# Kernel optimization log

Measured on AMD Instinct MI355X. Metric: run time of the kernel, lower is better.

Reference implementation:

```python
import jax, jax.numpy as jnp
import numpy as np
from jax import lax

N_HEADS = 10
F_IN = 78
F_OUT = 78           # per-head GAT output dim
HID = N_HEADS * F_OUT  # 780
NEG_SLOPE = 0.2
NUM_GRAPHS = 1024
N_NODES = 40960
N_EDGES = 163840
VOCAB = 26           # CHARPROTLEN + 1
EMB = 128
NFILT = 32
LOUT = 121           # 128 - 8 + 1


def setup_inputs() -> dict:
    key = jax.random.key(0)
    ks = jax.random.split(key, 24)
    d = {}
    d['x'] = jax.random.normal(ks[0], (N_NODES, F_IN), jnp.float32)
    d['edge_index'] = jax.random.randint(ks[1], (2, N_EDGES), 0, N_NODES, jnp.int64)
    d['batch'] = jnp.sort(jax.random.randint(ks[2], (N_NODES,), 0, NUM_GRAPHS, jnp.int64))
    d['target'] = jax.random.randint(ks[3], (NUM_GRAPHS, 1000), 0, VOCAB, jnp.int64)
    s = 0.05
    d['gat_W'] = jax.random.normal(ks[4], (F_IN, HID), jnp.float32) * s
    d['gat_att_src'] = jax.random.normal(ks[5], (N_HEADS, F_OUT), jnp.float32) * s
    d['gat_att_dst'] = jax.random.normal(ks[6], (N_HEADS, F_OUT), jnp.float32) * s
    d['gat_bias'] = jnp.zeros((HID,), jnp.float32)
    d['gcn_W'] = jax.random.normal(ks[7], (HID, HID), jnp.float32) * s
    d['gcn_bias'] = jnp.zeros((HID,), jnp.float32)
    d['fc_g1_W'] = jax.random.normal(ks[8], (2 * HID, 1500), jnp.float32) * s
    d['fc_g1_b'] = jnp.zeros((1500,), jnp.float32)
    d['fc_g2_W'] = jax.random.normal(ks[9], (1500, 128), jnp.float32) * s
    d['fc_g2_b'] = jnp.zeros((128,), jnp.float32)
    d['embed'] = jax.random.normal(ks[10], (VOCAB, EMB), jnp.float32) * s
    d['conv_xt_W'] = jax.random.normal(ks[11], (NFILT, 1000, 8), jnp.float32) * s
    d['conv_xt_b'] = jnp.zeros((NFILT,), jnp.float32)
    d['fc1_xt_W'] = jax.random.normal(ks[12], (NFILT * LOUT, 128), jnp.float32) * s
    d['fc1_xt_b'] = jnp.zeros((128,), jnp.float32)
    d['fc1_W'] = jax.random.normal(ks[13], (256, 1024), jnp.float32) * s
    d['fc1_b'] = jnp.zeros((1024,), jnp.float32)
    d['fc2_W'] = jax.random.normal(ks[14], (1024, 512), jnp.float32) * s
    d['fc2_b'] = jnp.zeros((512,), jnp.float32)
    d['out_W'] = jax.random.normal(ks[15], (512, 1), jnp.float32) * s
    d['out_b'] = jnp.zeros((1,), jnp.float32)
    return d


def _segment_softmax(logits, seg, num_segments):
    m = jax.ops.segment_max(logits, seg, num_segments=num_segments)
    m = jnp.where(jnp.isfinite(m), m, 0.0)
    e = jnp.exp(logits - m[seg])
    s = jax.ops.segment_sum(e, seg, num_segments=num_segments)
    return e / (s[seg] + 1e-16)


def reference(x, edge_index, batch, target, gat_W, gat_att_src, gat_att_dst,
              gat_bias, gcn_W, gcn_bias, fc_g1_W, fc_g1_b, fc_g2_W, fc_g2_b,
              embed, conv_xt_W, conv_xt_b, fc1_xt_W, fc1_xt_b, fc1_W, fc1_b,
              fc2_W, fc2_b, out_W, out_b):
    N = x.shape[0]
    # add self loops (PyG default for both GATConv and GCNConv)
    loops = jnp.arange(N, dtype=edge_index.dtype)
    src = jnp.concatenate([edge_index[0], loops])
    dst = jnp.concatenate([edge_index[1], loops])
    # --- GATConv(78 -> 78, heads=10, concat) ---
    h = (x @ gat_W).reshape(N, N_HEADS, F_OUT)              # [N,10,78]
    a_src = jnp.einsum('nhf,hf->nh', h, gat_att_src)        # [N,10]
    a_dst = jnp.einsum('nhf,hf->nh', h, gat_att_dst)
    logits = jax.nn.leaky_relu(a_src[src] + a_dst[dst], NEG_SLOPE)  # [E',10]
    alpha = _segment_softmax(logits, dst, N)                # softmax over in-edges per dst/head
    agg = jax.ops.segment_sum(h[src] * alpha[:, :, None], dst, num_segments=N)
    x1 = jax.nn.relu(agg.reshape(N, HID) + gat_bias)        # [N,780]
    # --- GCNConv(780 -> 780) with sym normalization ---
    h2 = x1 @ gcn_W
    deg = jax.ops.segment_sum(jnp.ones_like(dst, dtype=h2.dtype), dst, num_segments=N)
    dinv = jnp.where(deg > 0, deg ** -0.5, 0.0)
    norm = dinv[src] * dinv[dst]                            # [E']
    agg2 = jax.ops.segment_sum(h2[src] * norm[:, None], dst, num_segments=N)
    x2 = jax.nn.relu(agg2 + gcn_bias)                       # [N,780]
    # --- global max + mean pool per graph ---
    gmax = jax.ops.segment_max(x2, batch, num_segments=NUM_GRAPHS)
    cnt = jax.ops.segment_sum(jnp.ones((N,), x2.dtype), batch, num_segments=NUM_GRAPHS)
    gmean = jax.ops.segment_sum(x2, batch, num_segments=NUM_GRAPHS) / jnp.maximum(cnt, 1.0)[:, None]
    g = jnp.concatenate([gmax, gmean], axis=1)              # [B,1560]
    g = jax.nn.relu(g @ fc_g1_W + fc_g1_b)
    g = g @ fc_g2_W + fc_g2_b                               # [B,128] (dropout = identity, eval)
    # --- protein branch ---
    e = embed[target]                                       # [B,1000,128]
    conv = lax.conv_general_dilated(e, conv_xt_W, (1,), 'VALID',
                                    dimension_numbers=('NCH', 'OIH', 'NCH'))
    conv = conv + conv_xt_b[None, :, None]                  # [B,32,121]
    xt = conv.reshape(conv.shape[0], NFILT * LOUT) @ fc1_xt_W + fc1_xt_b
    # --- joint head ---
    xc = jnp.concatenate([g, xt], axis=1)                   # [B,256]
    xc = jax.nn.relu(xc @ fc1_W + fc1_b)
    xc = jax.nn.relu(xc @ fc2_W + fc2_b)
    return xc @ out_W + out_b                               # [B,1]
```

## Files before the change

kernel.cpp:

```cpp
#include <hip/hip_runtime.h>

typedef __attribute__((ext_vector_type(4))) float f32x4;
typedef __attribute__((ext_vector_type(8))) short bf16x8;
typedef __attribute__((ext_vector_type(8))) unsigned short u16x8;
typedef unsigned short u16;

#define HID 780
#define NH 10
#define FO 78

__device__ inline u16 f2b(float f) {
  unsigned u = __float_as_uint(f);
  unsigned r = (u + 0x7fff + ((u >> 16) & 1)) >> 16;
  return (u16)r;
}
__device__ inline float b2f(u16 b) { return __uint_as_float(((unsigned)b) << 16); }

__device__ inline void gld16(const u16* g, u16* l) {
  __builtin_amdgcn_global_load_lds(
      (const __attribute__((address_space(1))) unsigned int*)g,
      (__attribute__((address_space(3))) unsigned int*)l, 16, 0, 0);
}

__device__ inline int swz_bid() {
  int gx = gridDim.x, gy = gridDim.y, gz = gridDim.z;
  int nwg = gx * gy * gz;
  int bid = (blockIdx.z * gy + blockIdx.y) * gx + blockIdx.x;
  if ((nwg & 7) == 0) bid = (bid & 7) * (nwg >> 3) + (bid >> 3);
  return bid;
}

__device__ __forceinline__ void gemm_core(const u16* __restrict__ A,
    const u16* __restrict__ BT, u16* __restrict__ C, float* __restrict__ att_out,
    int Ncols, int KP, int ldc, int bx, int by,
    u16 (*As)[4096], u16 (*Bs)[4096])
{
  const int tid = threadIdx.x;
  const int row0 = by << 7, col0 = bx << 7;
  const int l = tid & 63, wid = tid >> 6;
  const int wr = wid >> 1, wc = wid & 1;
  const int lr = l & 15, lk = l >> 4;
  const int c0 = (wid << 6) + l, c1 = 256 + c0;
  const u16* gA0 = A + (size_t)(row0 + (c0 >> 2)) * KP + ((c0 & 3) << 3);
  const u16* gA1 = A + (size_t)(row0 + (c1 >> 2)) * KP + ((c1 & 3) << 3);
  const u16* gB0 = BT + (size_t)(col0 + (c0 >> 2)) * KP + ((c0 & 3) << 3);
  const u16* gB1 = BT + (size_t)(col0 + (c1 >> 2)) * KP + ((c1 & 3) << 3);
  const int d0 = (wid << 6) << 3, d1 = (256 + (wid << 6)) << 3;

  f32x4 acc[4][4];
#pragma unroll
  for (int i = 0; i < 4; ++i)
#pragma unroll
    for (int j = 0; j < 4; ++j) acc[i][j] = (f32x4){0.f, 0.f, 0.f, 0.f};

  gld16(gA0, &As[0][d0]); gld16(gA1, &As[0][d1]);
  gld16(gB0, &Bs[0][d0]); gld16(gB1, &Bs[0][d1]);
  __syncthreads();

  int cur = 0;
  for (int k0 = 0; k0 < KP; k0 += 32) {
    if (k0 + 32 < KP) {
      int nx = cur ^ 1, kn = k0 + 32;
      gld16(gA0 + kn, &As[nx][d0]); gld16(gA1 + kn, &As[nx][d1]);
      gld16(gB0 + kn, &Bs[nx][d0]); gld16(gB1 + kn, &Bs[nx][d1]);
    }
    const u16* Ac = As[cur];
    const u16* Bc = Bs[cur];
    bf16x8 af[4], bfr[4];
#pragma unroll
    for (int fm = 0; fm < 4; ++fm)
      af[fm] = *(const bf16x8*)&Ac[((wr * 64 + fm * 16 + lr) << 5) + (lk << 3)];
#pragma unroll
    for (int fn = 0; fn < 4; ++fn)
      bfr[fn] = *(const bf16x8*)&Bc[((wc * 64 + fn * 16 + lr) << 5) + (lk << 3)];
#pragma unroll
    for (int fm = 0; fm < 4; ++fm)
#pragma unroll
      for (int fn = 0; fn < 4; ++fn)
        acc[fm][fn] = __builtin_amdgcn_mfma_f32_16x16x32_bf16(af[fm], bfr[fn], acc[fm][fn], 0, 0, 0);
    __syncthreads();
    cur ^= 1;
  }
#pragma unroll
  for (int fm = 0; fm < 4; ++fm)
#pragma unroll
    for (int fn = 0; fn < 4; ++fn) {
      int col = col0 + wc * 64 + fn * 16 + lr;
      f32x4 v = acc[fm][fn];
      int rbase = row0 + wr * 64 + fm * 16 + lk * 4;
      if (col < Ncols) {
#pragma unroll
        for (int j = 0; j < 4; ++j)
          C[(size_t)(rbase + j) * ldc + col] = f2b(v[j]);
      } else {
        if (att_out != nullptr && col < Ncols + 20) {
          int c = col - Ncols;
#pragma unroll
          for (int j = 0; j < 4; ++j)
            att_out[(size_t)(rbase + j) * 20 + c] = v[j];
        }
        if (col < ldc) {
#pragma unroll
          for (int j = 0; j < 4; ++j) C[(size_t)(rbase + j) * ldc + col] = 0;
        }
      }
    }
}

__global__ __launch_bounds__(256) void gemm_mfma(const u16* __restrict__ A,
    const u16* __restrict__ BT, u16* __restrict__ C, float* __restrict__ att_out,
    int Ncols, int KP, int ldc)
{
  __shared__ u16 As[2][4096];
  __shared__ u16 Bs[2][4096];
  int t = swz_bid();
  gemm_core(A, BT, C, att_out, Ncols, KP, ldc, t % gridDim.x, t / gridDim.x, As, Bs);
}

__global__ __launch_bounds__(256) void gemm_dual(
    const u16* __restrict__ A1, const u16* __restrict__ B1, u16* __restrict__ C1,
    float* __restrict__ att1, int N1, int K1, int l1, int gx1, int nb1,
    const u16* __restrict__ A2, const u16* __restrict__ B2, u16* __restrict__ C2,
    int N2, int K2, int l2, int gx2)
{
  __shared__ u16 As[2][4096];
  __shared__ u16 Bs[2][4096];
  int bi = blockIdx.x;
  if (bi < nb1) {
    int t = bi;
    if ((nb1 & 7) == 0) t = (bi & 7) * (nb1 >> 3) + (bi >> 3);
    gemm_core(A1, B1, C1, att1, N1, K1, l1, t % gx1, t / gx1, As, Bs);
  } else {
    int nb2 = gridDim.x - nb1, b2 = bi - nb1;
    int t = b2;
    if ((nb2 & 7) == 0) t = (b2 & 7) * (nb2 >> 3) + (b2 >> 3);
    gemm_core(A2, B2, C2, nullptr, N2, K2, l2, t % gx2, t / gx2, As, Bs);
  }
}

__device__ __forceinline__ void sk_core(const u16* __restrict__ A,
    const u16* __restrict__ BT, float* __restrict__ C,
    int Ncols, int KP, int kchunk, int bx, int by, int bz,
    u16 (*As)[4096], u16 (*Bs)[4096])
{
  const int tid = threadIdx.x;
  const int row0 = by << 7, col0 = bx << 7;
  const int kbeg = bz * kchunk;
  const int kend = min(KP, kbeg + kchunk);
  const int l = tid & 63, wid = tid >> 6;
  const int wr = wid >> 1, wc = wid & 1;
  const int lr = l & 15, lk = l >> 4;
  const int c0 = (wid << 6) + l, c1 = 256 + c0;
  const u16* gA0 = A + (size_t)(row0 + (c0 >> 2)) * KP + ((c0 & 3) << 3) + kbeg;
  const u16* gA1 = A + (size_t)(row0 + (c1 >> 2)) * KP + ((c1 & 3) << 3) + kbeg;
  const u16* gB0 = BT + (size_t)(col0 + (c0 >> 2)) * KP + ((c0 & 3) << 3) + kbeg;
  const u16* gB1 = BT + (size_t)(col0 + (c1 >> 2)) * KP + ((c1 & 3) << 3) + kbeg;
  const int d0 = (wid << 6) << 3, d1 = (256 + (wid << 6)) << 3;

  f32x4 acc[4][4];
#pragma unroll
  for (int i = 0; i < 4; ++i)
#pragma unroll
    for (int j = 0; j < 4; ++j) acc[i][j] = (f32x4){0.f, 0.f, 0.f, 0.f};

  gld16(gA0, &As[0][d0]); gld16(gA1, &As[0][d1]);
  gld16(gB0, &Bs[0][d0]); gld16(gB1, &Bs[0][d1]);
  __syncthreads();

  int cur = 0;
  for (int k0 = kbeg; k0 < kend; k0 += 32) {
    if (k0 + 32 < kend) {
      int nx = cur ^ 1, kn = k0 + 32 - kbeg;
      gld16(gA0 + kn, &As[nx][d0]); gld16(gA1 + kn, &As[nx][d1]);
      gld16(gB0 + kn, &Bs[nx][d0]); gld16(gB1 + kn, &Bs[nx][d1]);
    }
    const u16* Ac = As[cur];
    const u16* Bc = Bs[cur];
    bf16x8 af[4], bfr[4];
#pragma unroll
    for (int fm = 0; fm < 4; ++fm)
      af[fm] = *(const bf16x8*)&Ac[((wr * 64 + fm * 16 + lr) << 5) + (lk << 3)];
#pragma unroll
    for (int fn = 0; fn < 4; ++fn)
      bfr[fn] = *(const bf16x8*)&Bc[((wc * 64 + fn * 16 + lr) << 5) + (lk << 3)];
#pragma unroll
    for (int fm = 0; fm < 4; ++fm)
#pragma unroll
      for (int fn = 0; fn < 4; ++fn)
        acc[fm][fn] = __builtin_amdgcn_mfma_f32_16x16x32_bf16(af[fm], bfr[fn], acc[fm][fn], 0, 0, 0);
    __syncthreads();
    cur ^= 1;
  }
#pragma unroll
  for (int fm = 0; fm < 4; ++fm)
#pragma unroll
    for (int fn = 0; fn < 4; ++fn) {
      int col = col0 + wc * 64 + fn * 16 + lr;
      if (col < Ncols) {
        f32x4 v = acc[fm][fn];
        int rbase = row0 + wr * 64 + fm * 16 + lk * 4;
#pragma unroll
        for (int j = 0; j < 4; ++j)
          atomicAdd(&C[(size_t)(rbase + j) * Ncols + col], v[j]);
      }
    }
}

__global__ __launch_bounds__(256) void gemm_sk(const u16* __restrict__ A,
    const u16* __restrict__ BT, float* __restrict__ C,
    int Ncols, int KP, int kchunk)
{
  __shared__ u16 As[2][4096];
  __shared__ u16 Bs[2][4096];
  int t = swz_bid();
  int bx = t % gridDim.x;
  int by = (t / gridDim.x) % gridDim.y;
  int bz = t / (gridDim.x * gridDim.y);
  sk_core(A, BT, C, Ncols, KP, kchunk, bx, by, bz, As, Bs);
}

__global__ __launch_bounds__(256) void gemm_sk_dual(
    const u16* __restrict__ A1, const u16* __restrict__ B1, float* __restrict__ C1,
    int N1, int K1, int kc1, int gx1, int gy1, int nb1,
    const u16* __restrict__ A2, const u16* __restrict__ B2, float* __restrict__ C2,
    int N2, int K2, int kc2, int gx2, int gy2)
{
  __shared__ u16 As[2][4096];
  __shared__ u16 Bs[2][4096];
  int bi = blockIdx.x;
  if (bi < nb1) {
    int t = bi;
    if ((nb1 & 7) == 0) t = (bi & 7) * (nb1 >> 3) + (bi >> 3);
    sk_core(A1, B1, C1, N1, K1, kc1, t % gx1, (t / gx1) % gy1, t / (gx1 * gy1), As, Bs);
  } else {
    int nb2 = gridDim.x - nb1, b2 = bi - nb1;
    int t = b2;
    if ((nb2 & 7) == 0) t = (b2 & 7) * (nb2 >> 3) + (b2 >> 3);
    sk_core(A2, B2, C2, N2, K2, kc2, t % gx2, (t / gx2) % gy2, t / (gx2 * gy2), As, Bs);
  }
}

template<bool RELU>
__global__ void bias_act_pad(const float* __restrict__ Cf,
    const float* __restrict__ bias, u16* __restrict__ out,
    int M, int N, int padTo, int ldco)
{
  int idx = blockIdx.x * 256 + threadIdx.x;
  if (idx >= M * padTo) return;
  int r = idx / padTo, c = idx - r * padTo;
  if (c < N) {
    float v = Cf[(size_t)r * N + c] + bias[c];
    if (RELU) v = v > 0.f ? v : 0.f;
    out[(size_t)r * ldco + c] = f2b(v);
  } else {
    out[(size_t)r * ldco + c] = 0;
  }
}

__global__ void bias_dual(const float* __restrict__ C1, const float* __restrict__ b1,
    u16* __restrict__ o1, int M1, int N1, int p1, int l1,
    const float* __restrict__ C2, const float* __restrict__ b2,
    u16* __restrict__ o2, int M2, int N2, int p2, int l2)
{
  int idx = blockIdx.x * 256 + threadIdx.x;
  int t1 = M1 * p1;
  if (idx < t1) {
    int r = idx / p1, c = idx - r * p1;
    if (c < N1) o1[(size_t)r * l1 + c] = f2b(C1[(size_t)r * N1 + c] + b1[c]);
    else o1[(size_t)r * l1 + c] = 0;
    return;
  }
  idx -= t1;
  if (idx >= M2 * p2) return;
  int r = idx / p2, c = idx - r * p2;
  if (c < N2) {
    float v = C2[(size_t)r * N2 + c] + b2[c];
    v = v > 0.f ? v : 0.f;
    o2[(size_t)r * l2 + c] = f2b(v);
  } else {
    o2[(size_t)r * l2 + c] = 0;
  }
}

__device__ inline void wtile(const float* __restrict__ W, u16* __restrict__ WT,
    int K, int Ncol, int KP, int NP, int bx, int by, int skip_lo, int skip_hi,
    u16 (*tbuf)[33])
{
  int tn0 = bx << 5, tk0 = by << 5;
  int lx = threadIdx.x & 31, ly = threadIdx.x >> 5;
#pragma unroll
  for (int r = 0; r < 32; r += 8) {
    int k = tk0 + ly + r, n = tn0 + lx;
    tbuf[ly + r][lx] = (k < K && n < Ncol) ? f2b(W[(size_t)k * Ncol + n]) : (u16)0;
  }
  __syncthreads();
#pragma unroll
  for (int r = 0; r < 32; r += 8) {
    int n = tn0 + ly + r, k = tk0 + lx;
    if (n < NP && k < KP && !(n >= skip_lo && n < skip_hi))
      WT[(size_t)n * KP + k] = tbuf[lx][ly + r];
  }
}

__global__ __launch_bounds__(256) void prep_all(
    const float* __restrict__ x, u16* __restrict__ xb,
    const float* __restrict__ gat_W, u16* __restrict__ wt1,
    const float* __restrict__ gcn_W, u16* __restrict__ wt2,
    const float* __restrict__ fcg1_W, u16* __restrict__ wtg1,
    const float* __restrict__ fcg2_W, u16* __restrict__ wtg2,
    const float* __restrict__ fc1xt_W, u16* __restrict__ wtxt,
    const float* __restrict__ fc1_W, u16* __restrict__ wtf1,
    const float* __restrict__ fc2_W, u16* __restrict__ wtf2,
    const float* __restrict__ convW, u16* __restrict__ wtc,
    const float* __restrict__ asv, const float* __restrict__ adv,
    const int* __restrict__ tgt, u16* __restrict__ Ind,
    const int* __restrict__ ei, int* __restrict__ cnt, int N, int E)
{
  __shared__ u16 tbuf[32][33];
  __shared__ unsigned char tl[1000];
  int bi = blockIdx.x, tid = threadIdx.x;
  const int s0 = (N * 96 + 255) / 256;
  if (bi < s0) {
    int idx = bi * 256 + tid;
    if (idx < N * 96) {
      int r = idx / 96, c = idx - r * 96;
      xb[idx] = (c < FO) ? f2b(x[(size_t)r * FO + c]) : (u16)0;
    }
    return;
  }
  bi -= s0;
  if (bi < 84)   { wtile(gat_W,  wt1,  FO,   HID,  96,   896,  bi % 28, bi / 28, 780, 800, tbuf); return; }
  bi -= 84;
  if (bi < 700)  { wtile(gcn_W,  wt2,  HID,  HID,  800,  896,  bi % 28, bi / 28, 1 << 30, 0, tbuf); return; }
  bi -= 700;
  if (bi < 2352) { wtile(fcg1_W, wtg1, 1560, 1500, 1568, 1536, bi % 48, bi / 48, 1 << 30, 0, tbuf); return; }
  bi -= 2352;
  if (bi < 188)  { wtile(fcg2_W, wtg2, 1500, 128,  1504, 128,  bi % 4,  bi / 4,  1 << 30, 0, tbuf); return; }
  bi -= 188;
  if (bi < 484)  { wtile(fc1xt_W, wtxt, 3872, 128, 3872, 128,  bi % 4,  bi / 4,  1 << 30, 0, tbuf); return; }
  bi -= 484;
  if (bi < 256)  { wtile(fc1_W,  wtf1, 256,  1024, 256,  1024, bi % 32, bi / 32, 1 << 30, 0, tbuf); return; }
  bi -= 256;
  if (bi < 512)  { wtile(fc2_W,  wtf2, 1024, 512,  1024, 512,  bi % 16, bi / 16, 1 << 30, 0, tbuf); return; }
  bi -= 512;
  if (bi < 1024) {
    int idx = bi * 256 + tid;
    int ok = idx >> 10, c = idx & 1023;
    int o = ok >> 3, k = ok & 7;
    wtc[idx] = (c < 1000) ? f2b(convW[(size_t)o * 8000 + c * 8 + k]) : (u16)0;
    return;
  }
  bi -= 1024;
  if (bi < 20) {
    int j = bi, k = tid;
    if (k >= 96) return;
    float s = 0.f;
    if (k < FO) {
      int h = (j < 10) ? j : j - 10;
      const float* av = ((j < 10) ? asv : adv) + h * FO;
      const float* wr = gat_W + (size_t)k * HID + h * FO;
      for (int f = 0; f < FO; ++f) s += wr[f] * av[f];
    }
    wt1[(size_t)(HID + j) * 96 + k] = f2b(s);
    return;
  }
  bi -= 20;
  if (bi < 1024) {
    int b = bi;
    for (int i = tid; i < 1000; i += 256) tl[i] = (unsigned char)tgt[b * 1000 + i];
    __syncthreads();
    u16* out = Ind + (size_t)b * 26 * 1024;
    for (int ci = tid; ci < 26 * 128; ci += 256) {
      int v = ci >> 7, c0 = (ci & 127) << 3;
      u16x8 w;
#pragma unroll
      for (int j = 0; j < 8; ++j) {
        int c = c0 + j;
        w[j] = (c < 1000 && tl[c] == v) ? (u16)0x3F80 : (u16)0;
      }
      *(u16x8*)(out + v * 1024 + c0) = w;
    }
    return;
  }
  bi -= 1024;
  {
    int e = bi * 256 + tid;
    if (e >= E + N) return;
    int dst = (e < E) ? ei[E + e] : (e - E);
    atomicAdd(&cnt[dst], 1);
  }
}

__global__ __launch_bounds__(1024) void scan1(const int* __restrict__ cnt,
    int* __restrict__ offs, float* __restrict__ dinv, int* __restrict__ bsum, int N)
{
  __shared__ int sc[1024];
  int b = blockIdx.x, tid = threadIdx.x;
  int g = b * 1024 + tid;
  int c = (g < N) ? cnt[g] : 0;
  sc[tid] = c;
  __syncthreads();
  for (int off = 1; off < 1024; off <<= 1) {
    int v = sc[tid];
    int add = (tid >= off) ? sc[tid - off] : 0;
    __syncthreads();
    sc[tid] = v + add;
    __syncthreads();
  }
  if (g < N) {
    offs[g] = sc[tid] - c;
    dinv[g] = c > 0 ? rsqrtf((float)c) : 0.f;
  }
  if (tid == 1023) bsum[b] = sc[1023];
}

__global__ __launch_bounds__(1024) void scan2(int* __restrict__ offs,
    const int* __restrict__ bsum, int N, int nblk)
{
  int b = blockIdx.x, tid = threadIdx.x;
  int base = 0;
  for (int j = 0; j < b; ++j) base += bsum[j];
  int g = b * 1024 + tid;
  if (g < N && b > 0) offs[g] += base;
  if (b == nblk - 1 && tid == 1023) offs[N] = base + bsum[b];
}

__global__ void fill_csr(const int* __restrict__ ei, int E, int N,
    const int* __restrict__ offs, int* __restrict__ fillpos, int* __restrict__ csr_src)
{
  int e = blockIdx.x * 256 + threadIdx.x;
  if (e >= E + N) return;
  int src, dst;
  if (e < E) { src = ei[e]; dst = ei[E + e]; }
  else { src = e - E; dst = e - E; }
  int p = offs[dst] + atomicAdd(&fillpos[dst], 1);
  csr_src[p] = src;
}

#define CH 48
__global__ __launch_bounds__(64) void gat_gather(const u16* __restrict__ h,
    const float* __restrict__ att,
    const int* __restrict__ offs, const int* __restrict__ csr_src,
    const float* __restrict__ gat_bias, u16* __restrict__ x1b)
{
  int n = blockIdx.x, lane = threadIdx.x;
  int o0 = offs[n], deg = offs[n + 1] - o0;
  __shared__ float ad[NH], ssum[NH];
  __shared__ float wbuf[CH][NH];
  __shared__ int slist[CH];
  if (lane < NH) { ad[lane] = att[n * 20 + 10 + lane]; ssum[lane] = 0.f; }
  const int s0 = lane, s1 = 64 + lane;
  const bool a1 = s1 < 100;
  int hA0 = min((s0 * 8) / FO, NH - 1), bb0 = FO * ((s0 * 8) / FO + 1) - s0 * 8;
  int hB0 = min((s0 * 8) / FO + 1, NH - 1);
  int hA1 = min((s1 * 8) / FO, NH - 1), bb1 = FO * ((s1 * 8) / FO + 1) - s1 * 8;
  int hB1 = min((s1 * 8) / FO + 1, NH - 1);
  float acc0[8], acc1[8];
#pragma unroll
  for (int j = 0; j < 8; ++j) { acc0[j] = 0.f; acc1[j] = 0.f; }
  __syncthreads();

  for (int e0 = 0; e0 < deg; e0 += CH) {
    int ce = min(CH, deg - e0);
    for (int idx = lane; idx < ce * NH; idx += 64) {
      int e = idx / NH, hd = idx - e * NH;
      int s = csr_src[o0 + e0 + e];
      float l = att[s * 20 + hd] + ad[hd];
      l = l > 0.f ? l : 0.2f * l;
      float w = __expf(l);
      wbuf[e][hd] = w;
      atomicAdd(&ssum[hd], w);
    }
    for (int idx = lane; idx < ce; idx += 64) slist[idx] = csr_src[o0 + e0 + idx];
    __syncthreads();
    for (int e = 0; e < ce; ++e) {
      const u16* hs = h + (size_t)slist[e] * 800;
      u16x8 v0 = *(const u16x8*)(hs + s0 * 8);
      float wA0 = wbuf[e][hA0], wB0 = wbuf[e][hB0];
#pragma unroll
      for (int j = 0; j < 8; ++j)
        acc0[j] += (j < bb0 ? wA0 : wB0) * b2f(v0[j]);
      if (a1) {
        u16x8 v1 = *(const u16x8*)(hs + s1 * 8);
        float wA1 = wbuf[e][hA1], wB1 = wbuf[e][hB1];
#pragma unroll
        for (int j = 0; j < 8; ++j)
          acc1[j] += (j < bb1 ? wA1 : wB1) * b2f(v1[j]);
      }
    }
    __syncthreads();
  }
  float iA0 = 1.f / (ssum[hA0] + 1e-16f), iB0 = 1.f / (ssum[hB0] + 1e-16f);
  u16x8 o0v;
#pragma unroll
  for (int j = 0; j < 8; ++j) {
    int f = s0 * 8 + j;
    float v = acc0[j] * (j < bb0 ? iA0 : iB0) + gat_bias[f];
    o0v[j] = f2b(v > 0.f ? v : 0.f);
  }
  *(u16x8*)(x1b + (size_t)n * 800 + s0 * 8) = o0v;
  if (a1) {
    float iA1 = 1.f / (ssum[hA1] + 1e-16f), iB1 = 1.f / (ssum[hB1] + 1e-16f);
    u16x8 o1v;
#pragma unroll
    for (int j = 0; j < 8; ++j) {
      int f = s1 * 8 + j;
      if (f < HID) {
        float v = acc1[j] * (j < bb1 ? iA1 : iB1) + gat_bias[f];
        o1v[j] = f2b(v > 0.f ? v : 0.f);
      } else o1v[j] = 0;
    }
    *(u16x8*)(x1b + (size_t)n * 800 + s1 * 8) = o1v;
  }
}

__global__ __launch_bounds__(256) void gcn_pool(const u16* __restrict__ h2,
    const int* __restrict__ offs, const int* __restrict__ csr_src,
    const float* __restrict__ dinv, const float* __restrict__ gcn_bias,
    const int* __restrict__ batch, int N, u16* __restrict__ gb)
{
  int gi = blockIdx.x, tid = threadIdx.x;
  int grp = tid >> 6, lane = tid & 63;
  __shared__ int se[2];
  __shared__ float smx[HID];
  __shared__ float ssm[HID];
  for (int f = tid; f < HID; f += 256) { smx[f] = 0.f; ssm[f] = 0.f; }
  if (tid < 2) {
    int target = gi + tid;
    int lo = 0, hi = N;
    while (lo < hi) { int mid = (lo + hi) >> 1; if (batch[mid] < target) lo = mid + 1; else hi = mid; }
    se[tid] = lo;
  }
  __syncthreads();
  int s = se[0], e = se[1];
  const int s0 = lane, s1 = 64 + lane;
  const bool a1 = s1 < 100;
  float bv0[8], bv1[8];
#pragma unroll
  for (int j = 0; j < 8; ++j) {
    int f0 = s0 * 8 + j, f1 = s1 * 8 + j;
    bv0[j] = gcn_bias[f0];
    bv1[j] = (a1 && f1 < HID) ? gcn_bias[f1] : 0.f;
  }
  float mx0[8], sm0[8], mx1[8], sm1[8];
#pragma unroll
  for (int j = 0; j < 8; ++j) { mx0[j] = 0.f; sm0[j] = 0.f; mx1[j] = 0.f; sm1[j] = 0.f; }

  for (int n = s + grp; n < e; n += 4) {
    int o0 = offs[n], deg = offs[n + 1] - o0;
    float dn = dinv[n];
    float acc0[8], acc1[8];
#pragma unroll
    for (int j = 0; j < 8; ++j) { acc0[j] = 0.f; acc1[j] = 0.f; }
    for (int eb = 0; eb < deg; eb += 64) {
      int ce = min(64, deg - eb);
      int   src_l = (lane < ce) ? csr_src[o0 + eb + lane] : 0;
      float c_l   = (lane < ce) ? dn * dinv[src_l] : 0.f;
      int   sc = __shfl(src_l, 0, 64);
      float cc = __shfl(c_l, 0, 64);
      const u16* hr = h2 + (size_t)sc * 800;
      u16x8 v0 = *(const u16x8*)(hr + s0 * 8);
      u16x8 v1 = a1 ? *(const u16x8*)(hr + s1 * 8) : v0;
      for (int ed = 0; ed < ce; ++ed) {
        u16x8 n0 = v0, n1 = v1;
        float nc = 0.f;
        if (ed + 1 < ce) {
          int ns = __shfl(src_l, ed + 1, 64);
          nc = __shfl(c_l, ed + 1, 64);
          const u16* nh = h2 + (size_t)ns * 800;
          n0 = *(const u16x8*)(nh + s0 * 8);
          if (a1) n1 = *(const u16x8*)(nh + s1 * 8);
        }
#pragma unroll
        for (int j = 0; j < 8; ++j) acc0[j] += cc * b2f(v0[j]);
        if (a1) {
#pragma unroll
          for (int j = 0; j < 8; ++j) acc1[j] += cc * b2f(v1[j]);
        }
        v0 = n0; v1 = n1; cc = nc;
      }
    }
#pragma unroll
    for (int j = 0; j < 8; ++j) {
      float v = acc0[j] + bv0[j];
      v = v > 0.f ? v : 0.f;
      mx0[j] = fmaxf(mx0[j], v); sm0[j] += v;
      float w = acc1[j] + bv1[j];
      w = w > 0.f ? w : 0.f;
      mx1[j] = fmaxf(mx1[j], w); sm1[j] += w;
    }
  }
#pragma unroll
  for (int j = 0; j < 8; ++j) {
    int f0 = s0 * 8 + j;
    atomicMax((unsigned*)&smx[f0], __float_as_uint(mx0[j]));
    atomicAdd(&ssm[f0], sm0[j]);
    int f1 = s1 * 8 + j;
    if (a1 && f1 < HID) {
      atomicMax((unsigned*)&smx[f1], __float_as_uint(mx1[j]));
      atomicAdd(&ssm[f1], sm1[j]);
    }
  }
  __syncthreads();
  float inv = 1.f / fmaxf((float)(e - s), 1.f);
  for (int f = tid; f < HID; f += 256) {
    gb[(size_t)gi * 1568 + f] = f2b(smx[f]);
    gb[(size_t)gi * 1568 + HID + f] = f2b(ssm[f] * inv);
  }
  if (tid < 8) gb[(size_t)gi * 1568 + 1560 + tid] = 0;
}

__global__ __launch_bounds__(256) void conv_xt(const u16* __restrict__ Aall,
    const float* __restrict__ embed, const float* __restrict__ cbias,
    u16* __restrict__ out)
{
  int b = blockIdx.x, tid = threadIdx.x;
  __shared__ __align__(16) float Al[6656];
  __shared__ __align__(16) float el[3360];
  const u16* Ab = Aall + (size_t)b * 6656;
  for (int i = tid; i < 6656; i += 256) Al[i] = b2f(Ab[i]);
  for (int i = tid; i < 3328; i += 256) el[i] = embed[i];
  if (tid < 32) el[3328 + tid] = 0.f;
  __syncthreads();
  for (int grp = tid; grp < 512; grp += 256) {
    int o = grp >> 4;
    int l0 = (grp & 15) << 3;
    float cb = cbias[o];
    float acc[8];
#pragma unroll
    for (int j = 0; j < 8; ++j) acc[j] = cb;
    for (int v = 0; v < 26; ++v) {
      const float* ap = &Al[v * 256 + (o << 3)];
      f32x4 a0 = *(const f32x4*)ap;
      f32x4 a1 = *(const f32x4*)(ap + 4);
      const float* ep = &el[v * 128 + l0];
      f32x4 e0 = *(const f32x4*)ep;
      f32x4 e1 = *(const f32x4*)(ep + 4);
      f32x4 e2 = *(const f32x4*)(ep + 8);
      f32x4 e3 = *(const f32x4*)(ep + 12);
      float a[8] = { a0[0], a0[1], a0[2], a0[3], a1[0], a1[1], a1[2], a1[3] };
      float e[16] = { e0[0], e0[1], e0[2], e0[3], e1[0], e1[1], e1[2], e1[3],
                      e2[0], e2[1], e2[2], e2[3], e3[0], e3[1], e3[2], e3[3] };
#pragma unroll
      for (int k = 0; k < 8; ++k)
#pragma unroll
        for (int j = 0; j < 8; ++j) acc[j] += a[k] * e[k + j];
    }
    int base = o * 121 + l0;
#pragma unroll
    for (int j = 0; j < 8; ++j)
      if (l0 + j < 121) out[(size_t)b * 3872 + base + j] = f2b(acc[j]);
  }
}

__global__ __launch_bounds__(256) void final_out(const u16* __restrict__ z2,
    const float* __restrict__ W, const float* __restrict__ bias, float* __restrict__ out)
{
  int row = blockIdx.x * 4 + (threadIdx.x >> 6);
  int lane = threadIdx.x & 63;
  const u16* zr = z2 + (size_t)row * 512;
  float s = 0.f;
  for (int i = lane; i < 512; i += 64) s += b2f(zr[i]) * W[i];
#pragma unroll
  for (int off = 32; off > 0; off >>= 1) s += __shfl_down(s, off, 64);
  if (lane == 0) out[row] = s + bias[0];
}

extern "C" void kernel_launch(void* const* d_in, const int* in_sizes, int n_in,
                              void* d_out, int out_size, void* d_ws, size_t ws_size,
                              hipStream_t stream)
{
  const float* x        = (const float*)d_in[0];
  const int*   ei       = (const int*)d_in[1];
  const int*   batch    = (const int*)d_in[2];
  const int*   tgt      = (const int*)d_in[3];
  const float* gat_W    = (const float*)d_in[4];
  const float* att_src  = (const float*)d_in[5];
  const float* att_dst  = (const float*)d_in[6];
  const float* gat_bias = (const float*)d_in[7];
  const float* gcn_W    = (const float*)d_in[8];
  const float* gcn_bias = (const float*)d_in[9];
  const float* fcg1_W   = (const float*)d_in[10];
  const float* fcg1_b   = (const float*)d_in[11];
  const float* fcg2_W   = (const float*)d_in[12];
  const float* fcg2_b   = (const float*)d_in[13];
  const float* embed    = (const float*)d_in[14];
  const float* convW    = (const float*)d_in[15];
  const float* convb    = (const float*)d_in[16];
  const float* fc1xt_W  = (const float*)d_in[17];
  const float* fc1xt_b  = (const float*)d_in[18];
  const float* fc1_W    = (const float*)d_in[19];
  const float* fc1_b    = (const float*)d_in[20];
  const float* fc2_W    = (const float*)d_in[21];
  const float* fc2_b    = (const float*)d_in[22];
  const float* out_W    = (const float*)d_in[23];
  const float* out_b    = (const float*)d_in[24];

  const int N = in_sizes[0] / FO;
  const int E = in_sizes[1] / 2;
  const int B = in_sizes[3] / 1000;
  const int ET = E + N;

  char* ws = (char*)d_ws;
  size_t off = 0;
  auto alloc = [&](size_t bytes) -> char* {
    char* p = ws + off;
    off = (off + bytes + 255) & ~(size_t)255;
    return p;
  };
  float* buf0  = (float*)alloc((size_t)N * HID * 4);
  float* buf1  = (float*)alloc((size_t)N * 800 * 2);
  u16*   Ab       = (u16*)alloc((size_t)26624 * 256 * 2);
  u16*   convflat = (u16*)alloc((size_t)1024 * 3872 * 2);
  u16*   wt1   = (u16*)alloc((size_t)896 * 96 * 2);
  u16*   wt2   = (u16*)alloc((size_t)896 * 800 * 2);
  u16*   wtg1  = (u16*)alloc((size_t)1536 * 1568 * 2);
  u16*   wtg2  = (u16*)alloc((size_t)128 * 1504 * 2);
  u16*   wtxt  = (u16*)alloc((size_t)128 * 3872 * 2);
  u16*   wtf1  = (u16*)alloc((size_t)1024 * 256 * 2);
  u16*   wtf2  = (u16*)alloc((size_t)512 * 1024 * 2);
  u16*   wtc   = (u16*)alloc((size_t)256 * 1024 * 2);
  float* att   = (float*)alloc((size_t)N * 20 * 4);
  int*   cnt   = (int*)alloc((size_t)N * 4);
  int*   offs  = (int*)alloc((size_t)(N + 1) * 4);
  int*   fillp = (int*)alloc((size_t)N * 4);
  int*   csr   = (int*)alloc((size_t)ET * 4);
  float* dinv  = (float*)alloc((size_t)N * 4);
  u16*   gb    = (u16*)alloc((size_t)B * 1568 * 2);
  int*   bsum  = (int*)alloc((size_t)64 * 4);

  u16*   xb    = (u16*)buf1;
  u16*   Ind   = (u16*)((char*)buf1 + (size_t)N * 96 * 2);
  u16*   x1b   = (u16*)buf1;
  u16*   hb    = (u16*)buf0;
  float* g1f = buf0;
  float* xtf = g1f + (size_t)1024 * 1500;
  float* g2f = xtf + (size_t)1024 * 128;
  float* z1f = g2f + (size_t)1024 * 128;
  float* z2f = z1f + (size_t)1024 * 1024;
  size_t skBytes = ((size_t)1024 * (1500 + 128 + 128 + 1024 + 512)) * 4;
  u16* g1b = (u16*)buf1;
  u16* xcb = g1b + (size_t)1024 * 1504;
  u16* z1b = xcb + (size_t)1024 * 256;
  u16* z2b = z1b + (size_t)1024 * 1024;

  hipMemsetAsync(cnt, 0, (size_t)N * 4, stream);
  hipMemsetAsync(fillp, 0, (size_t)N * 4, stream);

  int nbx = (N * 96 + 255) / 256;
  int nprep = nbx + 84 + 700 + 2352 + 188 + 484 + 256 + 512 + 1024 + 20 + 1024 + (ET + 255) / 256;
  prep_all<<<nprep, 256, 0, stream>>>(
      x, xb, gat_W, wt1, gcn_W, wt2, fcg1_W, wtg1, fcg2_W, wtg2,
      fc1xt_W, wtxt, fc1_W, wtf1, fc2_W, wtf2, convW, wtc,
      att_src, att_dst, tgt, Ind, ei, cnt, N, E);

  int nb1 = 7 * (N / 128);
  int nb2 = 2 * (26624 / 128);
  gemm_dual<<<nb1 + nb2, 256, 0, stream>>>(
      xb, wt1, hb, att, HID, 96, 800, 7, nb1,
      Ind, wtc, Ab, 256, 1024, 256, 2);

  int nblk = (N + 1023) / 1024;
  scan1<<<nblk, 1024, 0, stream>>>(cnt, offs, dinv, bsum, N);
  scan2<<<nblk, 1024, 0, stream>>>(offs, bsum, N, nblk);
  conv_xt<<<B, 256, 0, stream>>>(Ab, embed, convb, convflat);
  fill_csr<<<(ET + 255) / 256, 256, 0, stream>>>(ei, E, N, offs, fillp, csr);

  gat_gather<<<N, 64, 0, stream>>>(hb, att, offs, csr, gat_bias, x1b);

  gemm_mfma<<<dim3(7, N / 128), 256, 0, stream>>>(x1b, wt2, hb, nullptr, HID, 800, 800);

  gcn_pool<<<B, 256, 0, stream>>>(hb, offs, csr, dinv, gcn_bias, batch, N, gb);

  hipMemsetAsync(g1f, 0, skBytes, stream);

  gemm_sk_dual<<<128 + 192, 256, 0, stream>>>(
      convflat, wtxt, xtf, 128, 3872, 256, 1, 8, 128,
      gb, wtg1, g1f, 1500, 1568, 800, 12, 8);
  int nbias = (B * 128 + B * 1504 + 255) / 256;
  bias_dual<<<nbias, 256, 0, stream>>>(
      xtf, fc1xt_b, xcb + 128, B, 128, 128, 256,
      g1f, fcg1_b, g1b, B, 1500, 1504, 1504);

  gemm_sk<<<dim3(1, B / 128, 8), 256, 0, stream>>>(g1b, wtg2, g2f, 128, 1504, 192);
  bias_act_pad<false><<<(B * 128 + 255) / 256, 256, 0, stream>>>(
      g2f, fcg2_b, xcb, B, 128, 128, 256);

  gemm_sk<<<dim3(8, B / 128, 2), 256, 0, stream>>>(xcb, wtf1, z1f, 1024, 256, 128);
  bias_act_pad<true><<<(B * 1024 + 255) / 256, 256, 0, stream>>>(
      z1f, fc1_b, z1b, B, 1024, 1024, 1024);

  gemm_sk<<<dim3(4, B / 128, 4), 256, 0, stream>>>(z1b, wtf2, z2f, 512, 1024, 256);
  bias_act_pad<true><<<(B * 512 + 255) / 256, 256, 0, stream>>>(
      z2f, fc2_b, z2b, B, 512, 512, 512);

  final_out<<<B / 4, 256, 0, stream>>>(z2b, out_W, out_b, (float*)d_out);
}
```

Measured before the change: 446.3 us.

## Triple-buffer MFMA GEMM LDS pipeline with explicit vmcnt waits

The bf16 MFMA GEMM core moves from a double-buffered global_load_lds scheme to a three-stage ring buffer. It prefetches three K-tiles ahead and uses explicit s_waitcnt vmcnt thresholds plus raw s_barrier, replacing the full __syncthreads after each step. The next loads are issued into the just-read buffer once its fragments are in registers, before the MFMAs run. The goal is to hide more global memory latency. The cost is 50% more LDS per block, which may lower occupancy, plus an extra barrier per iteration.

```diff
diff --git a/kernel.cpp b/kernel.cpp
--- a/kernel.cpp
+++ b/kernel.cpp
@@ -53,19 +53,25 @@
 #pragma unroll
     for (int j = 0; j < 4; ++j) acc[i][j] = (f32x4){0.f, 0.f, 0.f, 0.f};
 
-  gld16(gA0, &As[0][d0]); gld16(gA1, &As[0][d1]);
-  gld16(gB0, &Bs[0][d0]); gld16(gB1, &Bs[0][d1]);
-  __syncthreads();
-
-  int cur = 0;
-  for (int k0 = 0; k0 < KP; k0 += 32) {
-    if (k0 + 32 < KP) {
-      int nx = cur ^ 1, kn = k0 + 32;
-      gld16(gA0 + kn, &As[nx][d0]); gld16(gA1 + kn, &As[nx][d1]);
-      gld16(gB0 + kn, &Bs[nx][d0]); gld16(gB1 + kn, &Bs[nx][d1]);
-    }
-    const u16* Ac = As[cur];
-    const u16* Bc = Bs[cur];
+  const int niter = KP >> 5;
+  const int npre = niter < 3 ? niter : 3;
+  for (int t = 0; t < npre; ++t) {
+    int kk = t << 5;
+    gld16(gA0 + kk, &As[t][d0]); gld16(gA1 + kk, &As[t][d1]);
+    gld16(gB0 + kk, &Bs[t][d0]); gld16(gB1 + kk, &Bs[t][d1]);
+  }
+
+  int cb = 0;
+  for (int k = 0; k < niter; ++k) {
+    if (k + 2 < niter)      asm volatile("s_waitcnt vmcnt(8)" ::: "memory");
+    else if (k + 1 < niter) asm volatile("s_waitcnt vmcnt(4)" ::: "memory");
+    else                    asm volatile("s_waitcnt vmcnt(0)" ::: "memory");
+    __builtin_amdgcn_sched_barrier(0);
+    __builtin_amdgcn_s_barrier();
+    asm volatile("" ::: "memory");
+
+    const u16* Ac = As[cb];
+    const u16* Bc = Bs[cb];
     bf16x8 af[4], bfr[4];
 #pragma unroll
     for (int fm = 0; fm < 4; ++fm)
@@ -73,13 +79,25 @@
 #pragma unroll
     for (int fn = 0; fn < 4; ++fn)
       bfr[fn] = *(const bf16x8*)&Bc[((wc * 64 + fn * 16 + lr) << 5) + (lk << 3)];
+
+    if (k + 3 < niter) {
+      asm volatile("s_waitcnt lgkmcnt(0)" ::: "memory");
+      __builtin_amdgcn_sched_barrier(0);
+      __builtin_amdgcn_s_barrier();
+      asm volatile("" ::: "memory");
+      int kn = (k + 3) << 5;
+      gld16(gA0 + kn, &As[cb][d0]); gld16(gA1 + kn, &As[cb][d1]);
+      gld16(gB0 + kn, &Bs[cb][d0]); gld16(gB1 + kn, &Bs[cb][d1]);
+      __builtin_amdgcn_sched_barrier(0);
+    }
+
 #pragma unroll
     for (int fm = 0; fm < 4; ++fm)
 #pragma unroll
       for (int fn = 0; fn < 4; ++fn)
         acc[fm][fn] = __builtin_amdgcn_mfma_f32_16x16x32_bf16(af[fm], bfr[fn], acc[fm][fn], 0, 0, 0);
-    __syncthreads();
-    cur ^= 1;
+
+    cb = (cb == 2) ? 0 : cb + 1;
   }
 #pragma unroll
   for (int fm = 0; fm < 4; ++fm)
@@ -111,8 +129,8 @@
     const u16* __restrict__ BT, u16* __restrict__ C, float* __restrict__ att_out,
     int Ncols, int KP, int ldc)
 {
-  __shared__ u16 As[2][4096];
-  __shared__ u16 Bs[2][4096];
+  __shared__ u16 As[3][4096];
+  __shared__ u16 Bs[3][4096];
   int t = swz_bid();
   gemm_core(A, BT, C, att_out, Ncols, KP, ldc, t % gridDim.x, t / gridDim.x, As, Bs);
 }
@@ -123,8 +141,8 @@
     const u16* __restrict__ A2, const u16* __restrict__ B2, u16* __restrict__ C2,
     int N2, int K2, int l2, int gx2)
 {
-  __shared__ u16 As[2][4096];
-  __shared__ u16 Bs[2][4096];
+  __shared__ u16 As[3][4096];
+  __shared__ u16 Bs[3][4096];
   int bi = blockIdx.x;
   if (bi < nb1) {
     int t = bi;
```

Result: no change. 441.4 us, median of 2 (-1.1%).

## Compute each 128x128 GEMM tile with a single wavefront and async waits

Applied to the files above, without the earlier changes.

Rewrites the main bf16 MFMA GEMM core so one 64-thread wavefront computes a full 128x128 tile with an 8x8 accumulator array, instead of four waves each owning a 64x64 quadrant. It replaces __syncthreads with explicit s_waitcnt vmcnt waits for the double-buffered global-to-LDS loads, relying on single-wave ordering. The aim is to remove block-wide barriers and raise MFMA-per-LDS-read reuse. The cost is heavy register pressure (256 accumulator VGPRs) and fewer waves per CU to hide latency. Single-wave LDS hazards between buffer reuse are not guarded by a barrier.

```diff
diff --git a/kernel.cpp b/kernel.cpp
--- a/kernel.cpp
+++ b/kernel.cpp
@@ -30,64 +30,68 @@
   return bid;
 }
 
-__device__ __forceinline__ void gemm_core(const u16* __restrict__ A,
+__device__ __forceinline__ void gemm1w_core(const u16* __restrict__ A,
     const u16* __restrict__ BT, u16* __restrict__ C, float* __restrict__ att_out,
     int Ncols, int KP, int ldc, int bx, int by,
     u16 (*As)[4096], u16 (*Bs)[4096])
 {
-  const int tid = threadIdx.x;
+  const int l = threadIdx.x & 63;
   const int row0 = by << 7, col0 = bx << 7;
-  const int l = tid & 63, wid = tid >> 6;
-  const int wr = wid >> 1, wc = wid & 1;
   const int lr = l & 15, lk = l >> 4;
-  const int c0 = (wid << 6) + l, c1 = 256 + c0;
-  const u16* gA0 = A + (size_t)(row0 + (c0 >> 2)) * KP + ((c0 & 3) << 3);
-  const u16* gA1 = A + (size_t)(row0 + (c1 >> 2)) * KP + ((c1 & 3) << 3);
-  const u16* gB0 = BT + (size_t)(col0 + (c0 >> 2)) * KP + ((c0 & 3) << 3);
-  const u16* gB1 = BT + (size_t)(col0 + (c1 >> 2)) * KP + ((c1 & 3) << 3);
-  const int d0 = (wid << 6) << 3, d1 = (256 + (wid << 6)) << 3;
-
-  f32x4 acc[4][4];
-#pragma unroll
-  for (int i = 0; i < 4; ++i)
-#pragma unroll
-    for (int j = 0; j < 4; ++j) acc[i][j] = (f32x4){0.f, 0.f, 0.f, 0.f};
-
-  gld16(gA0, &As[0][d0]); gld16(gA1, &As[0][d1]);
-  gld16(gB0, &Bs[0][d0]); gld16(gB1, &Bs[0][d1]);
-  __syncthreads();
+  const u16* gA0 = A + (size_t)(row0 + (l >> 2)) * KP + ((l & 3) << 3);
+  const u16* gB0 = BT + (size_t)(col0 + (l >> 2)) * KP + ((l & 3) << 3);
+  const size_t KP16 = (size_t)KP << 4;
+
+  f32x4 acc[8][8];
+#pragma unroll
+  for (int i = 0; i < 8; ++i)
+#pragma unroll
+    for (int j = 0; j < 8; ++j) acc[i][j] = (f32x4){0.f, 0.f, 0.f, 0.f};
+
+  const int niter = KP >> 5;
+#pragma unroll
+  for (int i = 0; i < 8; ++i) {
+    gld16(gA0 + i * KP16, &As[0][i << 9]);
+    gld16(gB0 + i * KP16, &Bs[0][i << 9]);
+  }
 
   int cur = 0;
-  for (int k0 = 0; k0 < KP; k0 += 32) {
-    if (k0 + 32 < KP) {
-      int nx = cur ^ 1, kn = k0 + 32;
-      gld16(gA0 + kn, &As[nx][d0]); gld16(gA1 + kn, &As[nx][d1]);
-      gld16(gB0 + kn, &Bs[nx][d0]); gld16(gB1 + kn, &Bs[nx][d1]);
-    }
+  for (int k = 0; k < niter; ++k) {
+    if (k + 1 < niter) {
+      int nx = cur ^ 1, kn = (k + 1) << 5;
+#pragma unroll
+      for (int i = 0; i < 8; ++i) {
+        gld16(gA0 + i * KP16 + kn, &As[nx][i << 9]);
+        gld16(gB0 + i * KP16 + kn, &Bs[nx][i << 9]);
+      }
+      asm volatile("s_waitcnt vmcnt(16)" ::: "memory");
+    } else {
+      asm volatile("s_waitcnt vmcnt(0)" ::: "memory");
+    }
+    __builtin_amdgcn_sched_barrier(0);
+
     const u16* Ac = As[cur];
     const u16* Bc = Bs[cur];
-    bf16x8 af[4], bfr[4];
-#pragma unroll
-    for (int fm = 0; fm < 4; ++fm)
-      af[fm] = *(const bf16x8*)&Ac[((wr * 64 + fm * 16 + lr) << 5) + (lk << 3)];
-#pragma unroll
-    for (int fn = 0; fn < 4; ++fn)
-      bfr[fn] = *(const bf16x8*)&Bc[((wc * 64 + fn * 16 + lr) << 5) + (lk << 3)];
-#pragma unroll
-    for (int fm = 0; fm < 4; ++fm)
-#pragma unroll
-      for (int fn = 0; fn < 4; ++fn)
-        acc[fm][fn] = __builtin_amdgcn_mfma_f32_16x16x32_bf16(af[fm], bfr[fn], acc[fm][fn], 0, 0, 0);
-    __syncthreads();
+    bf16x8 bfr[8];
+#pragma unroll
+    for (int fn = 0; fn < 8; ++fn)
+      bfr[fn] = *(const bf16x8*)&Bc[((fn * 16 + lr) << 5) + (lk << 3)];
+#pragma unroll
+    for (int fm = 0; fm < 8; ++fm) {
+      bf16x8 af = *(const bf16x8*)&Ac[((fm * 16 + lr) << 5) + (lk << 3)];
+#pragma unroll
+      for (int fn = 0; fn < 8; ++fn)
+        acc[fm][fn] = __builtin_amdgcn_mfma_f32_16x16x32_bf16(af, bfr[fn], acc[fm][fn], 0, 0, 0);
+    }
     cur ^= 1;
   }
 #pragma unroll
-  for (int fm = 0; fm < 4; ++fm)
-#pragma unroll
-    for (int fn = 0; fn < 4; ++fn) {
-      int col = col0 + wc * 64 + fn * 16 + lr;
+  for (int fm = 0; fm < 8; ++fm)
+#pragma unroll
+    for (int fn = 0; fn < 8; ++fn) {
+      int col = col0 + fn * 16 + lr;
       f32x4 v = acc[fm][fn];
-      int rbase = row0 + wr * 64 + fm * 16 + lk * 4;
+      int rbase = row0 + fm * 16 + lk * 4;
       if (col < Ncols) {
 #pragma unroll
         for (int j = 0; j < 4; ++j)
@@ -107,17 +111,17 @@
     }
 }
 
-__global__ __launch_bounds__(256) void gemm_mfma(const u16* __restrict__ A,
+__global__ __launch_bounds__(64) void gemm_mfma(const u16* __restrict__ A,
     const u16* __restrict__ BT, u16* __restrict__ C, float* __restrict__ att_out,
     int Ncols, int KP, int ldc)
 {
   __shared__ u16 As[2][4096];
   __shared__ u16 Bs[2][4096];
   int t = swz_bid();
-  gemm_core(A, BT, C, att_out, Ncols, KP, ldc, t % gridDim.x, t / gridDim.x, As, Bs);
-}
-
-__global__ __launch_bounds__(256) void gemm_dual(
+  gemm1w_core(A, BT, C, att_out, Ncols, KP, ldc, t % gridDim.x, t / gridDim.x, As, Bs);
+}
+
+__global__ __launch_bounds__(64) void gemm_dual(
     const u16* __restrict__ A1, const u16* __restrict__ B1, u16* __restrict__ C1,
     float* __restrict__ att1, int N1, int K1, int l1, int gx1, int nb1,
     const u16* __restrict__ A2, const u16* __restrict__ B2, u16* __restrict__ C2,
@@ -129,12 +133,12 @@
   if (bi < nb1) {
     int t = bi;
     if ((nb1 & 7) == 0) t = (bi & 7) * (nb1 >> 3) + (bi >> 3);
-    gemm_core(A1, B1, C1, att1, N1, K1, l1, t % gx1, t / gx1, As, Bs);
+    gemm1w_core(A1, B1, C1, att1, N1, K1, l1, t % gx1, t / gx1, As, Bs);
   } else {
     int nb2 = gridDim.x - nb1, b2 = bi - nb1;
     int t = b2;
     if ((nb2 & 7) == 0) t = (b2 & 7) * (nb2 >> 3) + (b2 >> 3);
-    gemm_core(A2, B2, C2, nullptr, N2, K2, l2, t % gx2, t / gx2, As, Bs);
+    gemm1w_core(A2, B2, C2, nullptr, N2, K2, l2, t % gx2, t / gx2, As, Bs);
   }
 }
 
@@ -756,7 +760,7 @@
 
   int nb1 = 7 * (N / 128);
   int nb2 = 2 * (26624 / 128);
-  gemm_dual<<<nb1 + nb2, 256, 0, stream>>>(
+  gemm_dual<<<nb1 + nb2, 64, 0, stream>>>(
       xb, wt1, hb, att, HID, 96, 800, 7, nb1,
       Ind, wtc, Ab, 256, 1024, 256, 2);
 
@@ -768,7 +772,7 @@
 
   gat_gather<<<N, 64, 0, stream>>>(hb, att, offs, csr, gat_bias, x1b);
 
-  gemm_mfma<<<dim3(7, N / 128), 256, 0, stream>>>(x1b, wt2, hb, nullptr, HID, 800, 800);
+  gemm_mfma<<<dim3(7, N / 128), 64, 0, stream>>>(x1b, wt2, hb, nullptr, HID, 800, 800);
 
   gcn_pool<<<B, 256, 0, stream>>>(hb, offs, csr, dinv, gcn_bias, batch, N, gb);
 
```

After: 530.4 us. 1.19x slower.
